# Performance work log

Measured on AMD Instinct MI355X. Metric: run time of the kernel, lower is better.

The kernel has to match this reference:

```python
import jax, jax.numpy as jnp
import numpy as np

DIM = 128
IND_DIM = 5
HEADS = 4
DIM_HEAD = 32
HIDDEN = HEADS * DIM_HEAD  # 128
SCALE = DIM_HEAD ** -0.5


def setup_inputs() -> dict:
    key = jax.random.key(0)
    ks = jax.random.split(key, 6)
    b, n = 1, 512
    x = jax.random.normal(ks[0], (b, DIM, n), dtype=jnp.float32)
    indicator = jax.random.normal(ks[1], (b, IND_DIM, n, n), dtype=jnp.float32)
    # conv1d kernels with kernel_size=1 are just (out, in) matrices
    w_qkv = jax.random.normal(ks[2], (HIDDEN * 3, DIM), dtype=jnp.float32) * (DIM ** -0.5)
    w_ind = jax.random.normal(ks[3], (HIDDEN * 2, IND_DIM), dtype=jnp.float32) * (IND_DIM ** -0.5)
    w_out = jax.random.normal(ks[4], (DIM, HIDDEN), dtype=jnp.float32) * (HIDDEN ** -0.5)
    b_out = jax.random.normal(ks[5], (DIM,), dtype=jnp.float32) * 0.01
    return {"x": x, "indicator": indicator, "w_qkv": w_qkv,
            "w_ind": w_ind, "w_out": w_out, "b_out": b_out}


def reference(x, indicator, w_qkv, w_ind, w_out, b_out):
    b, c, n = x.shape
    h, dh = HEADS, DIM_HEAD
    # pointwise conv = channel matmul
    qkv = jnp.einsum('oc,bcn->bon', w_qkv, x)  # (b, 3*hidden, n)
    q, k, v = jnp.split(qkv, 3, axis=1)
    q = q.reshape(b, h, dh, n)
    k = k.reshape(b, h, dh, n)
    v = v.reshape(b, h, dh, n)
    ind = jnp.einsum('oc,bcij->boij', w_ind, indicator)  # (b, 2*hidden, n, n)
    ind_q, ind_k = jnp.split(ind, 2, axis=1)
    ind_q = ind_q.reshape(b, h, dh, n, n)
    ind_k = ind_k.reshape(b, h, dh, n, n)
    qq = (q[..., :, None] + ind_q) * SCALE        # (b, h, dh, n, n)
    kk = k[..., None, :] + ind_k                   # (b, h, dh, n, n)
    sim = jnp.einsum('bhdij,bhdij->bhij', qq, kk)  # (b, h, n, n)
    attn = jax.nn.softmax(sim, axis=-1)
    out = jnp.einsum('bhij,bhdj->bhdi', attn, v)   # (b, h, dh, n)
    out = out.reshape(b, h * dh, n)
    return jnp.einsum('oc,bcn->bon', w_out, out) + b_out[None, :, None]
```

## Files before the change

kernel.cpp:

```cpp
#include <hip/hip_runtime.h>
#include <hip/hip_fp16.h>
#include <math.h>

#define N      512
#define DIMC   128
#define HEADS  4
#define DH     32
#define INDC   5
#define SCALE  0.1767766952966369f

#define QKV_ROWS 384
#define AQ_BASE  384
#define AK_BASE  404
#define TOT_ROWS 424
#define NROW_BLK (TOT_ROWS / 4)

#define MHS_F    (TOT_ROWS * N / 2)
#define WOUTT_F  (MHS_F + 64)

__global__ __launch_bounds__(256) void pre_kernel(const float* __restrict__ w_qkv,
                                                  const float* __restrict__ w_ind,
                                                  const float* __restrict__ x,
                                                  const float* __restrict__ w_out,
                                                  float* __restrict__ ws) {
    const int bx = blockIdx.x;
    const int t  = threadIdx.x;
    __half* rows  = (__half*)ws;
    float* MhS    = ws + MHS_F;
    float* w_outT = ws + WOUTT_F;

    if (bx == NROW_BLK) {
        if (blockIdx.y != 0) return;
        __shared__ float mraw[HEADS * INDC * INDC];
        if (t < HEADS * INDC * INDC) {
            const int h = t / 25, c = (t / 5) % 5, cc = t % 5;
            float acc = 0.f;
            for (int d = 0; d < DH; ++d)
                acc = fmaf(w_ind[(h * DH + d) * INDC + c],
                           w_ind[(DIMC + h * DH + d) * INDC + cc], acc);
            mraw[t] = acc;
        }
        __syncthreads();
        if (t < 64) {
            const int h = t >> 4, idx = t & 15;
            const int PC[10]  = {0, 0, 0, 0, 1, 1, 1, 2, 2, 3};
            const int PCC[10] = {1, 2, 3, 4, 2, 3, 4, 3, 4, 4};
            float s = 0.f;
            if (idx < 5) {
                s = mraw[h * 25 + idx * 5 + idx];
            } else if (idx < 15) {
                const int c = PC[idx - 5], cc = PCC[idx - 5];
                s = mraw[h * 25 + c * 5 + cc] + mraw[h * 25 + cc * 5 + c];
            }
            MhS[h * 16 + idx] = s;
        }
        for (int idx = t; idx < DIMC * DIMC; idx += 256) {
            const int o = idx >> 7, c = idx & 127;
            w_outT[c * DIMC + o] = w_out[idx];
        }
        return;
    }

    __shared__ float ws2[4 * DIMC];
    const int o0 = bx * 4;
    for (int idx = t; idx < 4 * DIMC; idx += 256) {
        const int r = idx & 3, m = idx >> 2;
        const int row = o0 + r;
        float val;
        if (row < QKV_ROWS) {
            val = w_qkv[row * DIMC + m];
        } else if (row < AK_BASE) {
            const int rr = row - AQ_BASE, h = rr / INDC, c = rr % INDC;
            float acc = 0.f;
            for (int d = 0; d < DH; ++d)
                acc = fmaf(w_qkv[(h * DH + d) * DIMC + m],
                           w_ind[(DIMC + h * DH + d) * INDC + c], acc);
            val = acc;
        } else {
            const int rr = row - AK_BASE, h = rr / INDC, c = rr % INDC;
            float acc = 0.f;
            for (int d = 0; d < DH; ++d)
                acc = fmaf(w_qkv[(DIMC + h * DH + d) * DIMC + m],
                           w_ind[(h * DH + d) * INDC + c], acc);
            val = acc;
        }
        ws2[m * 4 + r] = val;
    }
    __syncthreads();

    const int i = blockIdx.y * 256 + t;
    float acc[4] = {0.f, 0.f, 0.f, 0.f};
#pragma unroll 8
    for (int c = 0; c < DIMC; ++c) {
        const float xv = x[c * N + i];
        const float4 wv = *(const float4*)(ws2 + c * 4);
        acc[0] = fmaf(wv.x, xv, acc[0]);
        acc[1] = fmaf(wv.y, xv, acc[1]);
        acc[2] = fmaf(wv.z, xv, acc[2]);
        acc[3] = fmaf(wv.w, xv, acc[3]);
    }
#pragma unroll
    for (int r = 0; r < 4; ++r) rows[(o0 + r) * N + i] = __float2half(acc[r]);
}

__global__ __launch_bounds__(512) void attn_kernel(const float* __restrict__ ws,
                                                   const float* __restrict__ ind,
                                                   const float* __restrict__ b_out,
                                                   float* __restrict__ out) {
    const int i0   = blockIdx.x * 2;
    const int t    = threadIdx.x;
    const int lane = t & 63;
    const int w    = t >> 6;
    const int h    = w & 3;
    const int ii   = w >> 2;
    const int i    = i0 + ii;

    const __half* rows  = (const __half*)ws;
    const float* MhS    = ws + MHS_F;
    const float* w_outT = ws + WOUTT_F;

    __shared__ float qs[2][DIMC];
    __shared__ float aqs[2][HEADS * INDC];
    __shared__ float msS[HEADS * 16];
    __shared__ float red[8][DH][32];
    __shared__ float attv[2][DIMC];
    __shared__ float outred[8][2][DIMC];

    float4 ic[2][INDC];
#pragma unroll
    for (int s = 0; s < 2; ++s) {
        const int g = lane + 64 * s;
#pragma unroll
        for (int c = 0; c < INDC; ++c)
            ic[s][c] = ((const float4*)(ind + (c * N + i) * N))[g];
    }

    const __half* q  = rows;
    const __half* Aq = rows + 3 * DIMC * N;
    if (t < DIMC) {
        qs[0][t] = __half2float(q[t * N + i0]);
    } else if (t < 2 * DIMC) {
        qs[1][t - DIMC] = __half2float(q[(t - DIMC) * N + i0 + 1]);
    } else if (t < 2 * DIMC + 2 * HEADS * INDC) {
        const int r2 = t - 2 * DIMC;
        const int iw = r2 / (HEADS * INDC), r = r2 % (HEADS * INDC);
        aqs[iw][r] = __half2float(Aq[r * N + i0 + iw]);
    } else if (t < 2 * DIMC + 2 * HEADS * INDC + 64) {
        const int r = t - 2 * DIMC - 2 * HEADS * INDC;
        msS[r] = MhS[r];
    }
    __syncthreads();

    const float2* k4  = (const float2*)(rows + DIMC * N);
    const float2* v4  = (const float2*)(rows + 2 * DIMC * N);
    const float2* Ak4 = (const float2*)(rows + (3 * DIMC + HEADS * INDC) * N);

    float4 sr[2];
    float m = -1e30f;
#pragma unroll
    for (int s = 0; s < 2; ++s) {
        const int g = lane + 64 * s;
        float4 a = {0.f, 0.f, 0.f, 0.f};
#pragma unroll
        for (int d = 0; d < DH; ++d) {
            const float2 raw = k4[(h * DH + d) * 128 + g];
            const float2 fa = __half22float2(*(const __half2*)&raw.x);
            const float2 fb = __half22float2(*(const __half2*)&raw.y);
            const float qv = qs[ii][h * DH + d];
            a.x = fmaf(qv, fa.x, a.x); a.y = fmaf(qv, fa.y, a.y);
            a.z = fmaf(qv, fb.x, a.z); a.w = fmaf(qv, fb.y, a.w);
        }
#pragma unroll
        for (int c = 0; c < INDC; ++c) {
            const float2 raw = Ak4[(h * INDC + c) * 128 + g];
            const float2 fa = __half22float2(*(const __half2*)&raw.x);
            const float2 fb = __half22float2(*(const __half2*)&raw.y);
            const float b0 = aqs[ii][h * INDC + c];
            const float4 v0 = ic[s][c];
            a.x = fmaf(b0 + fa.x, v0.x, a.x); a.y = fmaf(b0 + fa.y, v0.y, a.y);
            a.z = fmaf(b0 + fb.x, v0.z, a.z); a.w = fmaf(b0 + fb.y, v0.w, a.w);
        }
        const int PCf[15]  = {0, 1, 2, 3, 4, 0, 0, 0, 0, 1, 1, 1, 2, 2, 3};
        const int PCCf[15] = {0, 1, 2, 3, 4, 1, 2, 3, 4, 2, 3, 4, 3, 4, 4};
#pragma unroll
        for (int p = 0; p < 15; ++p) {
            const float sv = msS[h * 16 + p];
            const float4 A = ic[s][PCf[p]], B = ic[s][PCCf[p]];
            a.x = fmaf(sv, A.x * B.x, a.x); a.y = fmaf(sv, A.y * B.y, a.y);
            a.z = fmaf(sv, A.z * B.z, a.z); a.w = fmaf(sv, A.w * B.w, a.w);
        }
        sr[s] = make_float4(SCALE * a.x, SCALE * a.y, SCALE * a.z, SCALE * a.w);
        m = fmaxf(m, fmaxf(fmaxf(sr[s].x, sr[s].y), fmaxf(sr[s].z, sr[s].w)));
    }

#pragma unroll
    for (int off = 1; off < 64; off <<= 1)
        m = fmaxf(m, __shfl_xor(m, off, 64));
    float4 e[2];
    float sum = 0.f;
#pragma unroll
    for (int s = 0; s < 2; ++s) {
        e[s].x = __expf(sr[s].x - m); e[s].y = __expf(sr[s].y - m);
        e[s].z = __expf(sr[s].z - m); e[s].w = __expf(sr[s].w - m);
        sum += (e[s].x + e[s].y) + (e[s].z + e[s].w);
    }
#pragma unroll
    for (int off = 1; off < 64; off <<= 1)
        sum += __shfl_xor(sum, off, 64);
    const float rnorm = 1.f / sum;

    float acc[DH];
#pragma unroll
    for (int d = 0; d < DH; ++d) acc[d] = 0.f;
#pragma unroll
    for (int s = 0; s < 2; ++s) {
        const int g = lane + 64 * s;
        const float4 p = e[s];
#pragma unroll
        for (int d = 0; d < DH; ++d) {
            const float2 raw = v4[(h * DH + d) * 128 + g];
            const float2 fa = __half22float2(*(const __half2*)&raw.x);
            const float2 fb = __half22float2(*(const __half2*)&raw.y);
            acc[d] = fmaf(p.x, fa.x, fmaf(p.y, fa.y,
                     fmaf(p.z, fb.x, fmaf(p.w, fb.y, acc[d]))));
        }
    }

    {
#pragma unroll
        for (int d = 0; d < DH; ++d)
            acc[d] += __shfl_xor(acc[d], 32, 64);
        const int l5 = lane & 31;
        if (lane < 32) {
#pragma unroll
            for (int dd = 0; dd < DH; ++dd) red[w][dd][l5 ^ dd] = acc[dd];
        }
        if (lane < 32) {
            float s = 0.f;
#pragma unroll
            for (int kk = 0; kk < 32; ++kk) s += red[w][l5][kk ^ l5];
            attv[ii][h * DH + l5] = s * rnorm;
        }
    }
    __syncthreads();

    {
        const int po  = t & 63;
        const int grp = t >> 6;
        const float2* wT2 = (const float2*)w_outT;
        float2 a0 = {0.f, 0.f}, a1 = {0.f, 0.f};
#pragma unroll
        for (int c = grp * 16; c < grp * 16 + 16; ++c) {
            const float2 wv = wT2[c * 64 + po];
            const float av0 = attv[0][c], av1 = attv[1][c];
            a0.x = fmaf(wv.x, av0, a0.x); a0.y = fmaf(wv.y, av0, a0.y);
            a1.x = fmaf(wv.x, av1, a1.x); a1.y = fmaf(wv.y, av1, a1.y);
        }
        ((float2*)&outred[grp][0][0])[po] = a0;
        ((float2*)&outred[grp][1][0])[po] = a1;
    }
    __syncthreads();
    if (t < 256) {
        const int o = t & 127, iw = t >> 7;
        float s = 0.f;
#pragma unroll
        for (int g = 0; g < 8; ++g) s += outred[g][iw][o];
        out[o * N + i0 + iw] = s + b_out[o];
    }
}

extern "C" void kernel_launch(void* const* d_in, const int* in_sizes, int n_in,
                              void* d_out, int out_size, void* d_ws, size_t ws_size,
                              hipStream_t stream) {
    const float* x         = (const float*)d_in[0];
    const float* indicator = (const float*)d_in[1];
    const float* w_qkv     = (const float*)d_in[2];
    const float* w_ind     = (const float*)d_in[3];
    const float* w_out     = (const float*)d_in[4];
    const float* b_out     = (const float*)d_in[5];
    float* out = (float*)d_out;
    float* ws  = (float*)d_ws;

    pre_kernel<<<dim3(NROW_BLK + 1, 2), 256, 0, stream>>>(w_qkv, w_ind, x, w_out, ws);
    attn_kernel<<<N / 2, 512, 0, stream>>>(ws, indicator, b_out, out);
}
```

Baseline: 98.88 us.

## Fuse projection prologue into attention kernel using cooperative grid sync

Merges the two launches into one cooperative kernel. Each block computes its own q/k/v and indicator-projection columns for its two positions, writes K/V rows to the workspace, then a grid-wide sync makes them visible before the attention phase. Q and the Aq terms stay in shared memory and skip the global round trip. This removes a launch and the inter-kernel gap, but every block redundantly recomputes the composed weights (about 5K dot products of length 32) and pays for a grid barrier; it also requires all 256 blocks to be co-resident.

New measurement: 235.8 us. +138.5%, slower.

```diff
diff --git a/kernel.cpp b/kernel.cpp
--- a/kernel.cpp
+++ b/kernel.cpp
@@ -1,6 +1,9 @@
 #include <hip/hip_runtime.h>
+#include <hip/hip_cooperative_groups.h>
 #include <hip/hip_fp16.h>
 #include <math.h>
+
+namespace cg = cooperative_groups;
 
 #define N      512
 #define DIMC   128
@@ -9,104 +12,18 @@
 #define INDC   5
 #define SCALE  0.1767766952966369f
 
-#define QKV_ROWS 384
-#define AQ_BASE  384
-#define AK_BASE  404
-#define TOT_ROWS 424
-#define NROW_BLK (TOT_ROWS / 4)
-
-#define MHS_F    (TOT_ROWS * N / 2)
-#define WOUTT_F  (MHS_F + 64)
-
-__global__ __launch_bounds__(256) void pre_kernel(const float* __restrict__ w_qkv,
-                                                  const float* __restrict__ w_ind,
-                                                  const float* __restrict__ x,
-                                                  const float* __restrict__ w_out,
-                                                  float* __restrict__ ws) {
-    const int bx = blockIdx.x;
-    const int t  = threadIdx.x;
-    __half* rows  = (__half*)ws;
-    float* MhS    = ws + MHS_F;
-    float* w_outT = ws + WOUTT_F;
-
-    if (bx == NROW_BLK) {
-        if (blockIdx.y != 0) return;
-        __shared__ float mraw[HEADS * INDC * INDC];
-        if (t < HEADS * INDC * INDC) {
-            const int h = t / 25, c = (t / 5) % 5, cc = t % 5;
-            float acc = 0.f;
-            for (int d = 0; d < DH; ++d)
-                acc = fmaf(w_ind[(h * DH + d) * INDC + c],
-                           w_ind[(DIMC + h * DH + d) * INDC + cc], acc);
-            mraw[t] = acc;
-        }
-        __syncthreads();
-        if (t < 64) {
-            const int h = t >> 4, idx = t & 15;
-            const int PC[10]  = {0, 0, 0, 0, 1, 1, 1, 2, 2, 3};
-            const int PCC[10] = {1, 2, 3, 4, 2, 3, 4, 3, 4, 4};
-            float s = 0.f;
-            if (idx < 5) {
-                s = mraw[h * 25 + idx * 5 + idx];
-            } else if (idx < 15) {
-                const int c = PC[idx - 5], cc = PCC[idx - 5];
-                s = mraw[h * 25 + c * 5 + cc] + mraw[h * 25 + cc * 5 + c];
-            }
-            MhS[h * 16 + idx] = s;
-        }
-        for (int idx = t; idx < DIMC * DIMC; idx += 256) {
-            const int o = idx >> 7, c = idx & 127;
-            w_outT[c * DIMC + o] = w_out[idx];
-        }
-        return;
-    }
-
-    __shared__ float ws2[4 * DIMC];
-    const int o0 = bx * 4;
-    for (int idx = t; idx < 4 * DIMC; idx += 256) {
-        const int r = idx & 3, m = idx >> 2;
-        const int row = o0 + r;
-        float val;
-        if (row < QKV_ROWS) {
-            val = w_qkv[row * DIMC + m];
-        } else if (row < AK_BASE) {
-            const int rr = row - AQ_BASE, h = rr / INDC, c = rr % INDC;
-            float acc = 0.f;
-            for (int d = 0; d < DH; ++d)
-                acc = fmaf(w_qkv[(h * DH + d) * DIMC + m],
-                           w_ind[(DIMC + h * DH + d) * INDC + c], acc);
-            val = acc;
-        } else {
-            const int rr = row - AK_BASE, h = rr / INDC, c = rr % INDC;
-            float acc = 0.f;
-            for (int d = 0; d < DH; ++d)
-                acc = fmaf(w_qkv[(DIMC + h * DH + d) * DIMC + m],
-                           w_ind[(h * DH + d) * INDC + c], acc);
-            val = acc;
-        }
-        ws2[m * 4 + r] = val;
-    }
-    __syncthreads();
-
-    const int i = blockIdx.y * 256 + t;
-    float acc[4] = {0.f, 0.f, 0.f, 0.f};
-#pragma unroll 8
-    for (int c = 0; c < DIMC; ++c) {
-        const float xv = x[c * N + i];
-        const float4 wv = *(const float4*)(ws2 + c * 4);
-        acc[0] = fmaf(wv.x, xv, acc[0]);
-        acc[1] = fmaf(wv.y, xv, acc[1]);
-        acc[2] = fmaf(wv.z, xv, acc[2]);
-        acc[3] = fmaf(wv.w, xv, acc[3]);
-    }
-#pragma unroll
-    for (int r = 0; r < 4; ++r) rows[(o0 + r) * N + i] = __float2half(acc[r]);
-}
-
-__global__ __launch_bounds__(512) void attn_kernel(const float* __restrict__ ws,
-                                                   const float* __restrict__ ind,
-                                                   const float* __restrict__ b_out,
-                                                   float* __restrict__ out) {
+#define KV_ROWS  276
+#define WOUTT_F  (KV_ROWS * N / 2)
+
+__global__ __launch_bounds__(512) void fused_kernel(
+        const float* __restrict__ x,
+        const float* __restrict__ ind,
+        const float* __restrict__ w_qkv,
+        const float* __restrict__ w_ind,
+        const float* __restrict__ w_out,
+        const float* __restrict__ b_out,
+        float* __restrict__ out,
+        float* __restrict__ ws) {
     const int i0   = blockIdx.x * 2;
     const int t    = threadIdx.x;
     const int lane = t & 63;
@@ -115,14 +32,16 @@
     const int ii   = w >> 2;
     const int i    = i0 + ii;
 
-    const __half* rows  = (const __half*)ws;
-    const float* MhS    = ws + MHS_F;
-    const float* w_outT = ws + WOUTT_F;
-
+    __half* rowsKV = (__half*)ws;
+    float*  w_outT = ws + WOUTT_F;
+
+    __shared__ float uni[8 * DH * 32];
+    float (*comp_w)[129] = (float (*)[129])uni;
+    __shared__ float xcol[2][DIMC];
     __shared__ float qs[2][DIMC];
     __shared__ float aqs[2][HEADS * INDC];
+    __shared__ float mraw[HEADS * INDC * INDC];
     __shared__ float msS[HEADS * 16];
-    __shared__ float red[8][DH][32];
     __shared__ float attv[2][DIMC];
     __shared__ float outred[8][2][DIMC];
 
@@ -135,25 +54,96 @@
             ic[s][c] = ((const float4*)(ind + (c * N + i) * N))[g];
     }
 
-    const __half* q  = rows;
-    const __half* Aq = rows + 3 * DIMC * N;
-    if (t < DIMC) {
-        qs[0][t] = __half2float(q[t * N + i0]);
-    } else if (t < 2 * DIMC) {
-        qs[1][t - DIMC] = __half2float(q[(t - DIMC) * N + i0 + 1]);
-    } else if (t < 2 * DIMC + 2 * HEADS * INDC) {
-        const int r2 = t - 2 * DIMC;
-        const int iw = r2 / (HEADS * INDC), r = r2 % (HEADS * INDC);
-        aqs[iw][r] = __half2float(Aq[r * N + i0 + iw]);
-    } else if (t < 2 * DIMC + 2 * HEADS * INDC + 64) {
-        const int r = t - 2 * DIMC - 2 * HEADS * INDC;
-        msS[r] = MhS[r];
-    }
-    __syncthreads();
-
-    const float2* k4  = (const float2*)(rows + DIMC * N);
-    const float2* v4  = (const float2*)(rows + 2 * DIMC * N);
-    const float2* Ak4 = (const float2*)(rows + (3 * DIMC + HEADS * INDC) * N);
+    if (t < 256) {
+        const int cc = t & 127, iw = t >> 7;
+        xcol[iw][cc] = x[cc * N + i0 + iw];
+    } else if (t < 356) {
+        const int u = t - 256, hh = u / 25, c = (u / 5) % 5, c2 = u % 5;
+        float acc = 0.f;
+        for (int d = 0; d < DH; ++d)
+            acc = fmaf(w_ind[(hh * DH + d) * INDC + c],
+                       w_ind[(DIMC + hh * DH + d) * INDC + c2], acc);
+        mraw[u] = acc;
+    }
+
+#pragma unroll
+    for (int k = 0; k < 10; ++k) {
+        const int idx = t + k * 512;
+        const int r = idx >> 7, m = idx & 127;
+        const int hh = (r % 20) / INDC, c = (r % 20) % INDC;
+        float acc = 0.f;
+        if (r < 20) {
+            for (int d = 0; d < DH; ++d)
+                acc = fmaf(w_qkv[(hh * DH + d) * DIMC + m],
+                           w_ind[(DIMC + hh * DH + d) * INDC + c], acc);
+        } else {
+            for (int d = 0; d < DH; ++d)
+                acc = fmaf(w_qkv[(DIMC + hh * DH + d) * DIMC + m],
+                           w_ind[(hh * DH + d) * INDC + c], acc);
+        }
+        comp_w[r][m] = acc;
+    }
+    __syncthreads();
+
+    if (t < 424) {
+        float a0 = 0.f, a1 = 0.f;
+        if (t < 384) {
+            const float* wr = w_qkv + t * DIMC;
+#pragma unroll 8
+            for (int c = 0; c < DIMC; ++c) {
+                const float wv = wr[c];
+                a0 = fmaf(wv, xcol[0][c], a0);
+                a1 = fmaf(wv, xcol[1][c], a1);
+            }
+        } else {
+            const float* wr = comp_w[t - 384];
+#pragma unroll 8
+            for (int c = 0; c < DIMC; ++c) {
+                const float wv = wr[c];
+                a0 = fmaf(wv, xcol[0][c], a0);
+                a1 = fmaf(wv, xcol[1][c], a1);
+            }
+        }
+        if (t < DIMC) {
+            qs[0][t] = a0; qs[1][t] = a1;
+        } else if (t < 384) {
+            const int r = t - DIMC;
+            __half2 h2; h2.x = __float2half(a0); h2.y = __float2half(a1);
+            *(__half2*)(rowsKV + r * N + i0) = h2;
+        } else if (t < 404) {
+            aqs[0][t - 384] = a0; aqs[1][t - 384] = a1;
+        } else {
+            const int r = 256 + (t - 404);
+            __half2 h2; h2.x = __float2half(a0); h2.y = __float2half(a1);
+            *(__half2*)(rowsKV + r * N + i0) = h2;
+        }
+    } else if (t < 488) {
+        const int idx = blockIdx.x * 64 + (t - 424);
+        const int c = idx >> 7, o = idx & 127;
+        w_outT[c * DIMC + o] = w_out[o * DIMC + c];
+    }
+    if (t >= 448) {
+        const int u = t - 448;
+        const int hh = u >> 4, idx = u & 15;
+        const int PC[10]  = {0, 0, 0, 0, 1, 1, 1, 2, 2, 3};
+        const int PCC[10] = {1, 2, 3, 4, 2, 3, 4, 3, 4, 4};
+        float s = 0.f;
+        if (idx < 5) {
+            s = mraw[hh * 25 + idx * 5 + idx];
+        } else if (idx < 15) {
+            const int c = PC[idx - 5], c2 = PCC[idx - 5];
+            s = mraw[hh * 25 + c * 5 + c2] + mraw[hh * 25 + c2 * 5 + c];
+        }
+        msS[hh * 16 + idx] = s;
+    }
+
+    __threadfence();
+    cg::this_grid().sync();
+    __threadfence();
+
+    const float2* k4  = (const float2*)(rowsKV);
+    const float2* v4  = (const float2*)(rowsKV + DIMC * N);
+    const float2* Ak4 = (const float2*)(rowsKV + 2 * DIMC * N);
 
     float4 sr[2];
     float m = -1e30f;
@@ -226,7 +216,9 @@
         }
     }
 
+    __syncthreads();
     {
+        float (*red)[DH][32] = (float (*)[DH][32])uni;
 #pragma unroll
         for (int d = 0; d < DH; ++d)
             acc[d] += __shfl_xor(acc[d], 32, 64);
@@ -234,8 +226,6 @@
         if (lane < 32) {
 #pragma unroll
             for (int dd = 0; dd < DH; ++dd) red[w][dd][l5 ^ dd] = acc[dd];
-        }
-        if (lane < 32) {
             float s = 0.f;
 #pragma unroll
             for (int kk = 0; kk < 32; ++kk) s += red[w][l5][kk ^ l5];
@@ -281,6 +271,8 @@
     float* out = (float*)d_out;
     float* ws  = (float*)d_ws;
 
-    pre_kernel<<<dim3(NROW_BLK + 1, 2), 256, 0, stream>>>(w_qkv, w_ind, x, w_out, ws);
-    attn_kernel<<<N / 2, 512, 0, stream>>>(ws, indicator, b_out, out);
+    void* args[] = {(void*)&x, (void*)&indicator, (void*)&w_qkv, (void*)&w_ind,
+                    (void*)&w_out, (void*)&b_out, (void*)&out, (void*)&ws};
+    hipLaunchCooperativeKernel((const void*)fused_kernel,
+                               dim3(N / 2), dim3(512), args, 0, stream);
 }
```
